# Optimization experiments

Hardware: AMD Instinct MI355X
Metric: run time of the kernel (lower is better)

The kernel has to match this reference:

```python
import jax, jax.numpy as jnp
import numpy as np

B, N, E, H = 2, 2048, 256, 8
D = E // H  # head dim = 32


def setup_inputs() -> dict:
    key = jax.random.key(0)
    ks = jax.random.split(key, 8)
    query_bbox = jax.random.uniform(ks[0], (B, N, 4), dtype=jnp.float32)
    query_feat = jax.random.normal(ks[1], (B, N, E), dtype=jnp.float32)
    s = 1.0 / np.sqrt(E)
    in_proj_w = jax.random.uniform(ks[2], (3 * E, E), minval=-s, maxval=s, dtype=jnp.float32)
    in_proj_b = jax.random.uniform(ks[3], (3 * E,), minval=-s, maxval=s, dtype=jnp.float32)
    out_proj_w = jax.random.uniform(ks[4], (E, E), minval=-s, maxval=s, dtype=jnp.float32)
    out_proj_b = jnp.zeros((E,), dtype=jnp.float32)
    # init_weights(): gen_tau weight zeroed, bias ~ U(0, 2)
    tau_w = jnp.zeros((H, E), dtype=jnp.float32)
    tau_b = jax.random.uniform(ks[5], (H,), minval=0.0, maxval=2.0, dtype=jnp.float32)
    return {
        "query_bbox": query_bbox,
        "query_feat": query_feat,
        "in_proj_w": in_proj_w,
        "in_proj_b": in_proj_b,
        "out_proj_w": out_proj_w,
        "out_proj_b": out_proj_b,
        "tau_w": tau_w,
        "tau_b": tau_b,
    }


def reference(query_bbox, query_feat, in_proj_w, in_proj_b, out_proj_w, out_proj_b, tau_w, tau_b):
    # pairwise center distances, negated; computed under no_grad in torch
    centers = query_bbox[..., :2]                                  # [B,N,2]
    diff = centers[:, :, None, :] - centers[:, None, :, :]         # [B,N,N,2]
    dist = -jnp.sqrt(jnp.sum(diff * diff, axis=-1))                # [B,N,N]
    dist = jax.lax.stop_gradient(dist)

    # per-head tau from query features
    tau = query_feat @ tau_w.T + tau_b                             # [B,N,H]
    tau = jnp.transpose(tau, (0, 2, 1))                            # [B,H,N]
    attn_mask = dist[:, None, :, :] * tau[..., None]               # [B,H,N,N]

    # multi-head self-attention (q = k = v = query_feat)
    qkv = query_feat @ in_proj_w.T + in_proj_b                     # [B,N,3E]
    q, k, v = jnp.split(qkv, 3, axis=-1)
    def heads(x):
        return jnp.transpose(x.reshape(B, N, H, D), (0, 2, 1, 3))  # [B,H,N,D]
    q, k, v = heads(q), heads(k), heads(v)

    scores = jnp.einsum("bhid,bhjd->bhij", q, k) / jnp.sqrt(jnp.float32(D))
    scores = scores + attn_mask
    attn = jax.nn.softmax(scores, axis=-1)                         # [B,H,N,N]
    o = jnp.einsum("bhij,bhjd->bhid", attn, v)                     # [B,H,N,D]
    o = jnp.transpose(o, (0, 2, 1, 3)).reshape(B, N, E)
    out = o @ out_proj_w.T + out_proj_b

    # mmcv MultiheadAttention adds the identity (residual); dropout in eval = id
    return query_feat + out
```

## Files before the change

kernel.cpp:

```cpp
#include <hip/hip_runtime.h>
#include <math.h>

#define BB 2
#define NN 2048
#define EE 256
#define HH 8
#define DD 32

typedef __attribute__((ext_vector_type(8))) short short8;
typedef __attribute__((ext_vector_type(4))) float f32x4;

__device__ inline unsigned short f2bf(float f) {
  union { float f; unsigned int u; } a; a.f = f;
  unsigned int r = a.u + 0x7FFFu + ((a.u >> 16) & 1u);
  return (unsigned short)(r >> 16);
}
__device__ inline float bf2f(short s) {
  union { unsigned int u; float f; } a;
  a.u = ((unsigned int)(unsigned short)s) << 16;
  return a.f;
}

__global__ __launch_bounds__(256) void cast_w_kernel(const float* __restrict__ in_w,
                                                     const float* __restrict__ out_w,
                                                     unsigned short* __restrict__ in_wb,
                                                     unsigned short* __restrict__ out_wb) {
  int i = blockIdx.x * 256 + threadIdx.x;
  float4 v;
  unsigned short* dst;
  if (i < 49152) {
    v = ((const float4*)in_w)[i];
    dst = in_wb + (size_t)i * 4;
  } else {
    v = ((const float4*)out_w)[i - 49152];
    dst = out_wb + (size_t)(i - 49152) * 4;
  }
  ushort4 u;
  u.x = f2bf(v.x); u.y = f2bf(v.y); u.z = f2bf(v.z); u.w = f2bf(v.w);
  *(ushort4*)dst = u;
}

__global__ __launch_bounds__(256) void tau_cxy_kernel(const float* __restrict__ feat,
                                                      const float* __restrict__ tau_w,
                                                      const float* __restrict__ tau_b,
                                                      const float* __restrict__ bbox,
                                                      float* __restrict__ tau2,
                                                      float2* __restrict__ cxy,
                                                      unsigned short* __restrict__ featb) {
  int idx = blockIdx.x * 256 + threadIdx.x;
  int row = idx >> 3, h = idx & 7;
  const float4* f = (const float4*)(feat + (size_t)row * EE);
  const float4* w = (const float4*)(tau_w + (size_t)h * EE);
  float s = 0.f;
#pragma unroll 8
  for (int e = 0; e < EE / 4; ++e) {
    float4 a = f[e], b4 = w[e];
    s = fmaf(a.x, b4.x, s);
    s = fmaf(a.y, b4.y, s);
    s = fmaf(a.z, b4.z, s);
    s = fmaf(a.w, b4.w, s);
    if ((e >> 3) == h) {
      ushort4 u;
      u.x = f2bf(a.x); u.y = f2bf(a.y); u.z = f2bf(a.z); u.w = f2bf(a.w);
      *(ushort4*)(featb + (size_t)row * EE + e * 4) = u;
    }
  }
  tau2[idx] = (s + tau_b[h]) * 1.4426950408889634f;
  if (h == 0) {
    float2 c;
    c.x = bbox[(size_t)row * 4 + 0];
    c.y = bbox[(size_t)row * 4 + 1];
    cxy[row] = c;
  }
}

__global__ __launch_bounds__(256) void dist_kernel(const float2* __restrict__ cxy,
                                                   unsigned short* __restrict__ nds) {
  int bq = blockIdx.x;
  int b = bq >> 7, qt = bq & 127;
  int tid = threadIdx.x;
  int w = tid >> 6, lane = tid & 63;
  int q15 = lane & 15, g = lane >> 4;
  int jt = blockIdx.y * 4 + w;

  float2 ci = cxy[b * NN + qt * 16 + q15];
  const float2* cb = cxy + b * NN + jt * 64;

  float nd[16];
#pragma unroll
  for (int t = 0; t < 4; ++t) {
    float4 c01 = *(const float4*)(cb + t * 16 + g * 4);
    float4 c23 = *(const float4*)(cb + t * 16 + g * 4 + 2);
    float cx[4] = {c01.x, c01.z, c23.x, c23.z};
    float cy[4] = {c01.y, c01.w, c23.y, c23.w};
#pragma unroll
    for (int r = 0; r < 4; ++r) {
      float dx = ci.x - cx[r], dy = ci.y - cy[r];
      nd[t * 4 + r] = -__builtin_amdgcn_sqrtf(fmaf(dy, dy, dx * dx));
    }
  }
  unsigned int u[8];
#pragma unroll
  for (int i = 0; i < 8; ++i)
    asm("v_cvt_pk_bf16_f32 %0, %1, %2" : "=v"(u[i]) : "v"(nd[2 * i]), "v"(nd[2 * i + 1]));
  unsigned short* dst = nds + ((size_t)(b * 128 + qt) * 32 + jt) * 1024 + lane * 16;
  *(uint4*)dst = make_uint4(u[0], u[1], u[2], u[3]);
  *(uint4*)(dst + 8) = make_uint4(u[4], u[5], u[6], u[7]);
}

template <int MODE>
__global__ __launch_bounds__(256) void gemm_mfma_kernel(const unsigned short* __restrict__ Ab,
                                                        const unsigned short* __restrict__ Wb,
                                                        const float* __restrict__ bias,
                                                        const float* __restrict__ resid,
                                                        float* __restrict__ Cf,
                                                        unsigned short* __restrict__ qb,
                                                        unsigned short* __restrict__ kh,
                                                        unsigned short* __restrict__ vpi) {
  int tid = threadIdx.x;
  int wv = tid >> 6, lane = tid & 63;
  int p = lane & 15, g = lane >> 4;
  int mW = blockIdx.y * 64 + wv * 16;
  int nB = blockIdx.x * 64;

  const unsigned short* ap = Ab + (size_t)(mW + p) * 256 + g * 8;
  const unsigned short* wp = Wb + (size_t)(nB + p) * 256 + g * 8;

  f32x4 acc[4] = {{0.f, 0.f, 0.f, 0.f}, {0.f, 0.f, 0.f, 0.f},
                  {0.f, 0.f, 0.f, 0.f}, {0.f, 0.f, 0.f, 0.f}};
#pragma unroll
  for (int kk = 0; kk < 8; ++kk) {
    short8 af = *(const short8*)(ap + kk * 32);
#pragma unroll
    for (int t = 0; t < 4; ++t) {
      short8 wf = *(const short8*)(wp + (size_t)t * 16 * 256 + kk * 32);
      acc[t] = __builtin_amdgcn_mfma_f32_16x16x32_bf16(af, wf, acc[t], 0, 0, 0);
    }
  }

#pragma unroll
  for (int t = 0; t < 4; ++t) {
    int n = nB + t * 16 + p;
    float bn = bias[n];
#pragma unroll
    for (int r = 0; r < 4; ++r) {
      int m = mW + g * 4 + r;
      float v = acc[t][r] + bn;
      if (MODE == 1) {
        Cf[(size_t)m * 256 + n] = v + resid[(size_t)m * 256 + n];
      } else {
        int b = m >> 11, tok = m & 2047;
        if (n < 256) {
          qb[(size_t)m * 256 + n] = f2bf(v * 0.25506659272582955f);
        } else if (n < 512) {
          int h = (n - 256) >> 5, d = n & 31;
          kh[((size_t)(b * 8 + h) * NN + tok) * 32 + d] = f2bf(v);
        } else {
          int h = (n - 512) >> 5, d = n & 31;
          int cp = ((tok & 15) << 1) | ((tok >> 4) & 1);
          vpi[(((size_t)(b * 8 + h) * 64 + (tok >> 5)) * 32 + d) * 32 + cp] = f2bf(v);
        }
      }
    }
  }
}

__global__ __launch_bounds__(256) void attn_kernel(const unsigned short* __restrict__ qb,
                                                   const unsigned short* __restrict__ kh,
                                                   const unsigned short* __restrict__ vpi,
                                                   const unsigned short* __restrict__ nds,
                                                   const float* __restrict__ tau2,
                                                   unsigned short* __restrict__ ob) {
  __shared__ float accT[4][32][17];
  __shared__ float lT[4][16];
  __shared__ float linv[16];

  int bh = blockIdx.y;
  int b = bh >> 3, h = bh & 7;
  int qtb = blockIdx.x;
  int tid = threadIdx.x;
  int w = tid >> 6;
  int lane = tid & 63;
  int q15 = lane & 15, g = lane >> 4;
  int rowq = b * NN + qtb * 16 + q15;

  short8 qf = *(const short8*)(qb + (size_t)rowq * 256 + h * 32 + g * 8);
  float t2 = tau2[(size_t)rowq * HH + h];

  float l = 0.f;
  f32x4 acc0 = {0.f, 0.f, 0.f, 0.f}, acc1 = {0.f, 0.f, 0.f, 0.f};

  const unsigned short* kb = kh + (size_t)bh * NN * 32 + q15 * 32 + g * 8;
  const unsigned short* vb = vpi + (size_t)bh * NN * 32 + q15 * 32 + g * 8;
  const unsigned short* ndb = nds + (size_t)(b * 128 + qtb) * 32 * 1024 + lane * 16;

  int j0base = w * 512;

  short8 kf[2][4];
  short8 vf[2][2];

#pragma unroll
  for (int t = 0; t < 4; ++t)
    kf[0][t] = *(const short8*)(kb + (size_t)(j0base + t * 16) * 32);

#pragma unroll
  for (int tt = 0; tt < 8; ++tt) {
    const int cur = tt & 1, nxt = cur ^ 1;
    const int j0 = j0base + tt * 64;
    const int jt = j0 >> 6;
    if (tt < 7) {
#pragma unroll
      for (int t = 0; t < 4; ++t)
        kf[nxt][t] = *(const short8*)(kb + (size_t)(j0 + 64 + t * 16) * 32);
    }
#pragma unroll
    for (int t2i = 0; t2i < 2; ++t2i)
#pragma unroll
      for (int dh = 0; dh < 2; ++dh)
        vf[t2i][dh] = *(const short8*)(vb + (size_t)((j0 >> 5) + t2i) * 1024 + dh * 512);
    short8 n0 = *(const short8*)(ndb + (size_t)jt * 1024);
    short8 n1 = *(const short8*)(ndb + (size_t)jt * 1024 + 8);
    f32x4 st[4];
#pragma unroll
    for (int t = 0; t < 4; ++t)
      st[t] = __builtin_amdgcn_mfma_f32_16x16x32_bf16(kf[cur][t], qf, (f32x4){0.f, 0.f, 0.f, 0.f}, 0, 0, 0);
    float p[16], lsum = 0.f;
#pragma unroll
    for (int i = 0; i < 16; ++i) {
      float ndf = bf2f(i < 8 ? n0[i] : n1[i - 8]);
      float e = fminf(fmaf(ndf, t2, st[i >> 2][i & 3]), 30.f);
      p[i] = __builtin_amdgcn_exp2f(e);
      lsum += p[i];
    }
    l += lsum;
    union { short8 v; unsigned int u[4]; } pf[2];
#pragma unroll
    for (int t2i = 0; t2i < 2; ++t2i)
#pragma unroll
      for (int wq = 0; wq < 4; ++wq) {
        float lo = p[t2i * 8 + wq];
        float hi = p[t2i * 8 + 4 + wq];
        asm("v_cvt_pk_bf16_f32 %0, %1, %2" : "=v"(pf[t2i].u[wq]) : "v"(lo), "v"(hi));
      }
    acc0 = __builtin_amdgcn_mfma_f32_16x16x32_bf16(vf[0][0], pf[0].v, acc0, 0, 0, 0);
    acc1 = __builtin_amdgcn_mfma_f32_16x16x32_bf16(vf[0][1], pf[0].v, acc1, 0, 0, 0);
    acc0 = __builtin_amdgcn_mfma_f32_16x16x32_bf16(vf[1][0], pf[1].v, acc0, 0, 0, 0);
    acc1 = __builtin_amdgcn_mfma_f32_16x16x32_bf16(vf[1][1], pf[1].v, acc1, 0, 0, 0);
  }

  l += __shfl_xor(l, 16);
  l += __shfl_xor(l, 32);

#pragma unroll
  for (int r = 0; r < 4; ++r) {
    accT[w][g * 4 + r][q15] = acc0[r];
    accT[w][16 + g * 4 + r][q15] = acc1[r];
  }
  if (g == 0) lT[w][q15] = l;
  __syncthreads();

  if (tid < 16) {
    float L = lT[0][tid] + lT[1][tid] + lT[2][tid] + lT[3][tid];
    linv[tid] = 1.f / fmaxf(L, 1e-30f);
  }
  __syncthreads();

#pragma unroll
  for (int ii = 0; ii < 2; ++ii) {
    int i = tid + ii * 256;
    int q = i >> 5, d = i & 31;
    float ov = (accT[0][d][q] + accT[1][d][q] + accT[2][d][q] + accT[3][d][q]) * linv[q];
    ob[((size_t)b * NN + qtb * 16 + q) * EE + h * 32 + d] = f2bf(ov);
  }
}

extern "C" void kernel_launch(void* const* d_in, const int* in_sizes, int n_in,
                              void* d_out, int out_size, void* d_ws, size_t ws_size,
                              hipStream_t stream) {
  const float* bbox  = (const float*)d_in[0];
  const float* feat  = (const float*)d_in[1];
  const float* in_w  = (const float*)d_in[2];
  const float* in_b  = (const float*)d_in[3];
  const float* out_w = (const float*)d_in[4];
  const float* out_b = (const float*)d_in[5];
  const float* tau_w = (const float*)d_in[6];
  const float* tau_b = (const float*)d_in[7];
  float* out = (float*)d_out;

  unsigned short* ob     = (unsigned short*)d_ws;
  unsigned short* featb  = ob + 1048576;
  unsigned short* qb     = featb + 1048576;
  unsigned short* kh     = qb + 1048576;
  unsigned short* vpi    = kh + 1048576;
  unsigned short* in_wb  = vpi + 1048576;
  unsigned short* out_wb = in_wb + 196608;
  float* tau2 = (float*)(out_wb + 65536);
  float2* cxy = (float2*)(tau2 + 32768);
  unsigned short* nds = (unsigned short*)(cxy + 4096);

  cast_w_kernel<<<dim3(256), 256, 0, stream>>>(in_w, out_w, in_wb, out_wb);
  tau_cxy_kernel<<<dim3(128), 256, 0, stream>>>(feat, tau_w, tau_b, bbox, tau2, cxy, featb);
  dist_kernel<<<dim3(BB * 128, 8), 256, 0, stream>>>(cxy, nds);
  gemm_mfma_kernel<0><<<dim3(12, 64), 256, 0, stream>>>(featb, in_wb, in_b, nullptr, nullptr,
                                                        qb, kh, vpi);
  attn_kernel<<<dim3(NN / 16, BB * HH), 256, 0, stream>>>(qb, kh, vpi, nds, tau2, ob);
  gemm_mfma_kernel<1><<<dim3(4, 64), 256, 0, stream>>>(ob, out_wb, out_b, feat, out,
                                                       nullptr, nullptr, nullptr);
}
```

Before: 92.64 us.

## Fuse prep kernels into one launch and process 32 queries per attention block

Three preprocessing kernels (weight cast, tau/feature cast, distance table) are merged into one kernel dispatched by block index, and the distance part now reads bbox centers directly, so the cxy buffer is gone. The attention kernel now handles two 16-query tiles per block, so each K and V fragment loaded is used for twice as many MFMAs, and the block count is halved. This removes two launches and halves K/V traffic per query. In exchange it raises register pressure and LDS use, and gives fewer blocks across the GPU.

```diff
diff --git a/kernel.cpp b/kernel.cpp
--- a/kernel.cpp
+++ b/kernel.cpp
@@ -21,91 +21,85 @@
   return a.f;
 }
 
-__global__ __launch_bounds__(256) void cast_w_kernel(const float* __restrict__ in_w,
-                                                     const float* __restrict__ out_w,
-                                                     unsigned short* __restrict__ in_wb,
-                                                     unsigned short* __restrict__ out_wb) {
-  int i = blockIdx.x * 256 + threadIdx.x;
-  float4 v;
-  unsigned short* dst;
-  if (i < 49152) {
-    v = ((const float4*)in_w)[i];
-    dst = in_wb + (size_t)i * 4;
+__global__ __launch_bounds__(256) void prep_kernel(const float* __restrict__ bbox,
+                                                   const float* __restrict__ feat,
+                                                   const float* __restrict__ in_w,
+                                                   const float* __restrict__ out_w,
+                                                   const float* __restrict__ tau_w,
+                                                   const float* __restrict__ tau_b,
+                                                   unsigned short* __restrict__ in_wb,
+                                                   unsigned short* __restrict__ out_wb,
+                                                   float* __restrict__ tau2,
+                                                   unsigned short* __restrict__ featb,
+                                                   unsigned short* __restrict__ nds) {
+  int blk = blockIdx.x;
+  int tid = threadIdx.x;
+  if (blk < 256) {
+    int i = blk * 256 + tid;
+    float4 v;
+    unsigned short* dst;
+    if (i < 49152) {
+      v = ((const float4*)in_w)[i];
+      dst = in_wb + (size_t)i * 4;
+    } else {
+      v = ((const float4*)out_w)[i - 49152];
+      dst = out_wb + (size_t)(i - 49152) * 4;
+    }
+    ushort4 u;
+    u.x = f2bf(v.x); u.y = f2bf(v.y); u.z = f2bf(v.z); u.w = f2bf(v.w);
+    *(ushort4*)dst = u;
+  } else if (blk < 384) {
+    int idx = (blk - 256) * 256 + tid;
+    int row = idx >> 3, h = idx & 7;
+    const float4* f = (const float4*)(feat + (size_t)row * EE);
+    const float4* w = (const float4*)(tau_w + (size_t)h * EE);
+    float s = 0.f;
+#pragma unroll 8
+    for (int e = 0; e < EE / 4; ++e) {
+      float4 a = f[e], b4 = w[e];
+      s = fmaf(a.x, b4.x, s);
+      s = fmaf(a.y, b4.y, s);
+      s = fmaf(a.z, b4.z, s);
+      s = fmaf(a.w, b4.w, s);
+      if ((e >> 3) == h) {
+        ushort4 u;
+        u.x = f2bf(a.x); u.y = f2bf(a.y); u.z = f2bf(a.z); u.w = f2bf(a.w);
+        *(ushort4*)(featb + (size_t)row * EE + e * 4) = u;
+      }
+    }
+    tau2[idx] = (s + tau_b[h]) * 1.4426950408889634f;
   } else {
-    v = ((const float4*)out_w)[i - 49152];
-    dst = out_wb + (size_t)(i - 49152) * 4;
-  }
-  ushort4 u;
-  u.x = f2bf(v.x); u.y = f2bf(v.y); u.z = f2bf(v.z); u.w = f2bf(v.w);
-  *(ushort4*)dst = u;
-}
-
-__global__ __launch_bounds__(256) void tau_cxy_kernel(const float* __restrict__ feat,
-                                                      const float* __restrict__ tau_w,
-                                                      const float* __restrict__ tau_b,
-                                                      const float* __restrict__ bbox,
-                                                      float* __restrict__ tau2,
-                                                      float2* __restrict__ cxy,
-                                                      unsigned short* __restrict__ featb) {
-  int idx = blockIdx.x * 256 + threadIdx.x;
-  int row = idx >> 3, h = idx & 7;
-  const float4* f = (const float4*)(feat + (size_t)row * EE);
-  const float4* w = (const float4*)(tau_w + (size_t)h * EE);
-  float s = 0.f;
-#pragma unroll 8
-  for (int e = 0; e < EE / 4; ++e) {
-    float4 a = f[e], b4 = w[e];
-    s = fmaf(a.x, b4.x, s);
-    s = fmaf(a.y, b4.y, s);
-    s = fmaf(a.z, b4.z, s);
-    s = fmaf(a.w, b4.w, s);
-    if ((e >> 3) == h) {
-      ushort4 u;
-      u.x = f2bf(a.x); u.y = f2bf(a.y); u.z = f2bf(a.z); u.w = f2bf(a.w);
-      *(ushort4*)(featb + (size_t)row * EE + e * 4) = u;
-    }
-  }
-  tau2[idx] = (s + tau_b[h]) * 1.4426950408889634f;
-  if (h == 0) {
-    float2 c;
-    c.x = bbox[(size_t)row * 4 + 0];
-    c.y = bbox[(size_t)row * 4 + 1];
-    cxy[row] = c;
-  }
-}
-
-__global__ __launch_bounds__(256) void dist_kernel(const float2* __restrict__ cxy,
-                                                   unsigned short* __restrict__ nds) {
-  int bq = blockIdx.x;
-  int b = bq >> 7, qt = bq & 127;
-  int tid = threadIdx.x;
-  int w = tid >> 6, lane = tid & 63;
-  int q15 = lane & 15, g = lane >> 4;
-  int jt = blockIdx.y * 4 + w;
-
-  float2 ci = cxy[b * NN + qt * 16 + q15];
-  const float2* cb = cxy + b * NN + jt * 64;
-
-  float nd[16];
-#pragma unroll
-  for (int t = 0; t < 4; ++t) {
-    float4 c01 = *(const float4*)(cb + t * 16 + g * 4);
-    float4 c23 = *(const float4*)(cb + t * 16 + g * 4 + 2);
-    float cx[4] = {c01.x, c01.z, c23.x, c23.z};
-    float cy[4] = {c01.y, c01.w, c23.y, c23.w};
-#pragma unroll
-    for (int r = 0; r < 4; ++r) {
-      float dx = ci.x - cx[r], dy = ci.y - cy[r];
-      nd[t * 4 + r] = -__builtin_amdgcn_sqrtf(fmaf(dy, dy, dx * dx));
-    }
-  }
-  unsigned int u[8];
-#pragma unroll
-  for (int i = 0; i < 8; ++i)
-    asm("v_cvt_pk_bf16_f32 %0, %1, %2" : "=v"(u[i]) : "v"(nd[2 * i]), "v"(nd[2 * i + 1]));
-  unsigned short* dst = nds + ((size_t)(b * 128 + qt) * 32 + jt) * 1024 + lane * 16;
-  *(uint4*)dst = make_uint4(u[0], u[1], u[2], u[3]);
-  *(uint4*)(dst + 8) = make_uint4(u[4], u[5], u[6], u[7]);
+    int blk2 = blk - 384;
+    int bq = blk2 >> 3;
+    int yy = blk2 & 7;
+    int b = bq >> 7, qt = bq & 127;
+    int w = tid >> 6, lane = tid & 63;
+    int q15 = lane & 15, g = lane >> 4;
+    int jt = yy * 4 + w;
+
+    const float* bi = bbox + (size_t)(b * NN + qt * 16 + q15) * 4;
+    float cix = bi[0], ciy = bi[1];
+    const float* bj = bbox + (size_t)(b * NN + jt * 64) * 4;
+
+    float nd[16];
+#pragma unroll
+    for (int t = 0; t < 4; ++t) {
+#pragma unroll
+      for (int r = 0; r < 4; ++r) {
+        int j = t * 16 + g * 4 + r;
+        float2 cj = *(const float2*)(bj + (size_t)j * 4);
+        float dx = cix - cj.x, dy = ciy - cj.y;
+        nd[t * 4 + r] = -__builtin_amdgcn_sqrtf(fmaf(dy, dy, dx * dx));
+      }
+    }
+    unsigned int u[8];
+#pragma unroll
+    for (int i = 0; i < 8; ++i)
+      asm("v_cvt_pk_bf16_f32 %0, %1, %2" : "=v"(u[i]) : "v"(nd[2 * i]), "v"(nd[2 * i + 1]));
+    unsigned short* dst = nds + ((size_t)(b * 128 + qt) * 32 + jt) * 1024 + lane * 16;
+    *(uint4*)dst = make_uint4(u[0], u[1], u[2], u[3]);
+    *(uint4*)(dst + 8) = make_uint4(u[4], u[5], u[6], u[7]);
+  }
 }
 
 template <int MODE>
@@ -171,9 +165,9 @@
                                                    const unsigned short* __restrict__ nds,
                                                    const float* __restrict__ tau2,
                                                    unsigned short* __restrict__ ob) {
-  __shared__ float accT[4][32][17];
-  __shared__ float lT[4][16];
-  __shared__ float linv[16];
+  __shared__ float accT[4][32][33];
+  __shared__ float lT[4][32];
+  __shared__ float linv[32];
 
   int bh = blockIdx.y;
   int b = bh >> 3, h = bh & 7;
@@ -182,17 +176,23 @@
   int w = tid >> 6;
   int lane = tid & 63;
   int q15 = lane & 15, g = lane >> 4;
-  int rowq = b * NN + qtb * 16 + q15;
-
-  short8 qf = *(const short8*)(qb + (size_t)rowq * 256 + h * 32 + g * 8);
-  float t2 = tau2[(size_t)rowq * HH + h];
-
-  float l = 0.f;
-  f32x4 acc0 = {0.f, 0.f, 0.f, 0.f}, acc1 = {0.f, 0.f, 0.f, 0.f};
+
+  int row0 = b * NN + qtb * 32 + q15;
+  int row1 = row0 + 16;
+
+  short8 qf0 = *(const short8*)(qb + (size_t)row0 * 256 + h * 32 + g * 8);
+  short8 qf1 = *(const short8*)(qb + (size_t)row1 * 256 + h * 32 + g * 8);
+  float t20 = tau2[(size_t)row0 * HH + h];
+  float t21 = tau2[(size_t)row1 * HH + h];
+
+  float l0 = 0.f, l1 = 0.f;
+  f32x4 acc00 = {0.f, 0.f, 0.f, 0.f}, acc01 = {0.f, 0.f, 0.f, 0.f};
+  f32x4 acc10 = {0.f, 0.f, 0.f, 0.f}, acc11 = {0.f, 0.f, 0.f, 0.f};
 
   const unsigned short* kb = kh + (size_t)bh * NN * 32 + q15 * 32 + g * 8;
   const unsigned short* vb = vpi + (size_t)bh * NN * 32 + q15 * 32 + g * 8;
-  const unsigned short* ndb = nds + (size_t)(b * 128 + qtb) * 32 * 1024 + lane * 16;
+  const unsigned short* ndb0 = nds + (size_t)(b * 128 + qtb * 2) * 32768 + lane * 16;
+  const unsigned short* ndb1 = ndb0 + 32768;
 
   int j0base = w * 512;
 
@@ -218,59 +218,82 @@
 #pragma unroll
       for (int dh = 0; dh < 2; ++dh)
         vf[t2i][dh] = *(const short8*)(vb + (size_t)((j0 >> 5) + t2i) * 1024 + dh * 512);
-    short8 n0 = *(const short8*)(ndb + (size_t)jt * 1024);
-    short8 n1 = *(const short8*)(ndb + (size_t)jt * 1024 + 8);
-    f32x4 st[4];
-#pragma unroll
-    for (int t = 0; t < 4; ++t)
-      st[t] = __builtin_amdgcn_mfma_f32_16x16x32_bf16(kf[cur][t], qf, (f32x4){0.f, 0.f, 0.f, 0.f}, 0, 0, 0);
-    float p[16], lsum = 0.f;
+    short8 na0 = *(const short8*)(ndb0 + (size_t)jt * 1024);
+    short8 na1 = *(const short8*)(ndb0 + (size_t)jt * 1024 + 8);
+    short8 nb0 = *(const short8*)(ndb1 + (size_t)jt * 1024);
+    short8 nb1 = *(const short8*)(ndb1 + (size_t)jt * 1024 + 8);
+
+    f32x4 st0[4], st1[4];
+#pragma unroll
+    for (int t = 0; t < 4; ++t) {
+      st0[t] = __builtin_amdgcn_mfma_f32_16x16x32_bf16(kf[cur][t], qf0, (f32x4){0.f, 0.f, 0.f, 0.f}, 0, 0, 0);
+      st1[t] = __builtin_amdgcn_mfma_f32_16x16x32_bf16(kf[cur][t], qf1, (f32x4){0.f, 0.f, 0.f, 0.f}, 0, 0, 0);
+    }
+    float p0[16], p1[16];
+    float ls0 = 0.f, ls1 = 0.f;
 #pragma unroll
     for (int i = 0; i < 16; ++i) {
-      float ndf = bf2f(i < 8 ? n0[i] : n1[i - 8]);
-      float e = fminf(fmaf(ndf, t2, st[i >> 2][i & 3]), 30.f);
-      p[i] = __builtin_amdgcn_exp2f(e);
-      lsum += p[i];
-    }
-    l += lsum;
-    union { short8 v; unsigned int u[4]; } pf[2];
+      float nda = bf2f(i < 8 ? na0[i] : na1[i - 8]);
+      float e0 = fminf(fmaf(nda, t20, st0[i >> 2][i & 3]), 30.f);
+      p0[i] = __builtin_amdgcn_exp2f(e0);
+      ls0 += p0[i];
+      float ndbv = bf2f(i < 8 ? nb0[i] : nb1[i - 8]);
+      float e1 = fminf(fmaf(ndbv, t21, st1[i >> 2][i & 3]), 30.f);
+      p1[i] = __builtin_amdgcn_exp2f(e1);
+      ls1 += p1[i];
+    }
+    l0 += ls0;
+    l1 += ls1;
+    union { short8 v; unsigned int u[4]; } pf0[2], pf1[2];
 #pragma unroll
     for (int t2i = 0; t2i < 2; ++t2i)
 #pragma unroll
       for (int wq = 0; wq < 4; ++wq) {
-        float lo = p[t2i * 8 + wq];
-        float hi = p[t2i * 8 + 4 + wq];
-        asm("v_cvt_pk_bf16_f32 %0, %1, %2" : "=v"(pf[t2i].u[wq]) : "v"(lo), "v"(hi));
+        asm("v_cvt_pk_bf16_f32 %0, %1, %2"
+            : "=v"(pf0[t2i].u[wq]) : "v"(p0[t2i * 8 + wq]), "v"(p0[t2i * 8 + 4 + wq]));
+        asm("v_cvt_pk_bf16_f32 %0, %1, %2"
+            : "=v"(pf1[t2i].u[wq]) : "v"(p1[t2i * 8 + wq]), "v"(p1[t2i * 8 + 4 + wq]));
       }
-    acc0 = __builtin_amdgcn_mfma_f32_16x16x32_bf16(vf[0][0], pf[0].v, acc0, 0, 0, 0);
-    acc1 = __builtin_amdgcn_mfma_f32_16x16x32_bf16(vf[0][1], pf[0].v, acc1, 0, 0, 0);
-    acc0 = __builtin_amdgcn_mfma_f32_16x16x32_bf16(vf[1][0], pf[1].v, acc0, 0, 0, 0);
-    acc1 = __builtin_amdgcn_mfma_f32_16x16x32_bf16(vf[1][1], pf[1].v, acc1, 0, 0, 0);
-  }
-
-  l += __shfl_xor(l, 16);
-  l += __shfl_xor(l, 32);
+    acc00 = __builtin_amdgcn_mfma_f32_16x16x32_bf16(vf[0][0], pf0[0].v, acc00, 0, 0, 0);
+    acc01 = __builtin_amdgcn_mfma_f32_16x16x32_bf16(vf[0][1], pf0[0].v, acc01, 0, 0, 0);
+    acc10 = __builtin_amdgcn_mfma_f32_16x16x32_bf16(vf[0][0], pf1[0].v, acc10, 0, 0, 0);
+    acc11 = __builtin_amdgcn_mfma_f32_16x16x32_bf16(vf[0][1], pf1[0].v, acc11, 0, 0, 0);
+    acc00 = __builtin_amdgcn_mfma_f32_16x16x32_bf16(vf[1][0], pf0[1].v, acc00, 0, 0, 0);
+    acc01 = __builtin_amdgcn_mfma_f32_16x16x32_bf16(vf[1][1], pf0[1].v, acc01, 0, 0, 0);
+    acc10 = __builtin_amdgcn_mfma_f32_16x16x32_bf16(vf[1][0], pf1[1].v, acc10, 0, 0, 0);
+    acc11 = __builtin_amdgcn_mfma_f32_16x16x32_bf16(vf[1][1], pf1[1].v, acc11, 0, 0, 0);
+  }
+
+  l0 += __shfl_xor(l0, 16);
+  l0 += __shfl_xor(l0, 32);
+  l1 += __shfl_xor(l1, 16);
+  l1 += __shfl_xor(l1, 32);
 
 #pragma unroll
   for (int r = 0; r < 4; ++r) {
-    accT[w][g * 4 + r][q15] = acc0[r];
-    accT[w][16 + g * 4 + r][q15] = acc1[r];
-  }
-  if (g == 0) lT[w][q15] = l;
+    accT[w][g * 4 + r][q15] = acc00[r];
+    accT[w][16 + g * 4 + r][q15] = acc01[r];
+    accT[w][g * 4 + r][16 + q15] = acc10[r];
+    accT[w][16 + g * 4 + r][16 + q15] = acc11[r];
+  }
+  if (g == 0) {
+    lT[w][q15] = l0;
+    lT[w][16 + q15] = l1;
+  }
   __syncthreads();
 
-  if (tid < 16) {
+  if (tid < 32) {
     float L = lT[0][tid] + lT[1][tid] + lT[2][tid] + lT[3][tid];
     linv[tid] = 1.f / fmaxf(L, 1e-30f);
   }
   __syncthreads();
 
 #pragma unroll
-  for (int ii = 0; ii < 2; ++ii) {
+  for (int ii = 0; ii < 4; ++ii) {
     int i = tid + ii * 256;
     int q = i >> 5, d = i & 31;
     float ov = (accT[0][d][q] + accT[1][d][q] + accT[2][d][q] + accT[3][d][q]) * linv[q];
-    ob[((size_t)b * NN + qtb * 16 + q) * EE + h * 32 + d] = f2bf(ov);
+    ob[((size_t)b * NN + qtb * 32 + q) * EE + h * 32 + d] = f2bf(ov);
   }
 }
 
@@ -295,15 +318,13 @@
   unsigned short* in_wb  = vpi + 1048576;
   unsigned short* out_wb = in_wb + 196608;
   float* tau2 = (float*)(out_wb + 65536);
-  float2* cxy = (float2*)(tau2 + 32768);
-  unsigned short* nds = (unsigned short*)(cxy + 4096);
-
-  cast_w_kernel<<<dim3(256), 256, 0, stream>>>(in_w, out_w, in_wb, out_wb);
-  tau_cxy_kernel<<<dim3(128), 256, 0, stream>>>(feat, tau_w, tau_b, bbox, tau2, cxy, featb);
-  dist_kernel<<<dim3(BB * 128, 8), 256, 0, stream>>>(cxy, nds);
+  unsigned short* nds = (unsigned short*)(tau2 + 32768);
+
+  prep_kernel<<<dim3(2432), 256, 0, stream>>>(bbox, feat, in_w, out_w, tau_w, tau_b,
+                                              in_wb, out_wb, tau2, featb, nds);
   gemm_mfma_kernel<0><<<dim3(12, 64), 256, 0, stream>>>(featb, in_wb, in_b, nullptr, nullptr,
                                                         qb, kh, vpi);
-  attn_kernel<<<dim3(NN / 16, BB * HH), 256, 0, stream>>>(qb, kh, vpi, nds, tau2, ob);
+  attn_kernel<<<dim3(NN / 32, BB * HH), 256, 0, stream>>>(qb, kh, vpi, nds, tau2, ob);
   gemm_mfma_kernel<1><<<dim3(4, 64), 256, 0, stream>>>(ob, out_wb, out_b, feat, out,
                                                        nullptr, nullptr, nullptr);
 }
```

Measured after the change: 82.27 us, median of 2. 11.2% less time.

## Compute pairwise distances inside attention and merge prep kernels into one launch

Applied to the files above, without the earlier changes.

Removes the separate distance kernel that wrote a bf16 [B,N,N] distance matrix and instead computes the negated center distances on the fly inside the attention loop from the cxy buffer. This drops a large global write plus the matching reads, and also merges the weight-cast and tau/cxy kernels into a single prep launch, removing launches. In exchange the attention kernel does 8x redundant sqrt work (once per head) and extra small loads of centers per tile. Precision changes slightly too, since distances are no longer rounded to bf16.

```diff
diff --git a/kernel.cpp b/kernel.cpp
--- a/kernel.cpp
+++ b/kernel.cpp
@@ -15,97 +15,61 @@
   unsigned int r = a.u + 0x7FFFu + ((a.u >> 16) & 1u);
   return (unsigned short)(r >> 16);
 }
-__device__ inline float bf2f(short s) {
-  union { unsigned int u; float f; } a;
-  a.u = ((unsigned int)(unsigned short)s) << 16;
-  return a.f;
-}
-
-__global__ __launch_bounds__(256) void cast_w_kernel(const float* __restrict__ in_w,
-                                                     const float* __restrict__ out_w,
-                                                     unsigned short* __restrict__ in_wb,
-                                                     unsigned short* __restrict__ out_wb) {
-  int i = blockIdx.x * 256 + threadIdx.x;
-  float4 v;
-  unsigned short* dst;
-  if (i < 49152) {
-    v = ((const float4*)in_w)[i];
-    dst = in_wb + (size_t)i * 4;
+
+__global__ __launch_bounds__(256) void prep_kernel(const float* __restrict__ bbox,
+                                                   const float* __restrict__ feat,
+                                                   const float* __restrict__ in_w,
+                                                   const float* __restrict__ out_w,
+                                                   const float* __restrict__ tau_w,
+                                                   const float* __restrict__ tau_b,
+                                                   unsigned short* __restrict__ in_wb,
+                                                   unsigned short* __restrict__ out_wb,
+                                                   float* __restrict__ tau2,
+                                                   unsigned short* __restrict__ featb,
+                                                   float2* __restrict__ cxy) {
+  int blk = blockIdx.x;
+  int tid = threadIdx.x;
+  if (blk < 256) {
+    int i = blk * 256 + tid;
+    float4 v;
+    unsigned short* dst;
+    if (i < 49152) {
+      v = ((const float4*)in_w)[i];
+      dst = in_wb + (size_t)i * 4;
+    } else {
+      v = ((const float4*)out_w)[i - 49152];
+      dst = out_wb + (size_t)(i - 49152) * 4;
+    }
+    ushort4 u;
+    u.x = f2bf(v.x); u.y = f2bf(v.y); u.z = f2bf(v.z); u.w = f2bf(v.w);
+    *(ushort4*)dst = u;
   } else {
-    v = ((const float4*)out_w)[i - 49152];
-    dst = out_wb + (size_t)(i - 49152) * 4;
-  }
-  ushort4 u;
-  u.x = f2bf(v.x); u.y = f2bf(v.y); u.z = f2bf(v.z); u.w = f2bf(v.w);
-  *(ushort4*)dst = u;
-}
-
-__global__ __launch_bounds__(256) void tau_cxy_kernel(const float* __restrict__ feat,
-                                                      const float* __restrict__ tau_w,
-                                                      const float* __restrict__ tau_b,
-                                                      const float* __restrict__ bbox,
-                                                      float* __restrict__ tau2,
-                                                      float2* __restrict__ cxy,
-                                                      unsigned short* __restrict__ featb) {
-  int idx = blockIdx.x * 256 + threadIdx.x;
-  int row = idx >> 3, h = idx & 7;
-  const float4* f = (const float4*)(feat + (size_t)row * EE);
-  const float4* w = (const float4*)(tau_w + (size_t)h * EE);
-  float s = 0.f;
+    int idx = (blk - 256) * 256 + tid;
+    int row = idx >> 3, h = idx & 7;
+    const float4* f = (const float4*)(feat + (size_t)row * EE);
+    const float4* w = (const float4*)(tau_w + (size_t)h * EE);
+    float s = 0.f;
 #pragma unroll 8
-  for (int e = 0; e < EE / 4; ++e) {
-    float4 a = f[e], b4 = w[e];
-    s = fmaf(a.x, b4.x, s);
-    s = fmaf(a.y, b4.y, s);
-    s = fmaf(a.z, b4.z, s);
-    s = fmaf(a.w, b4.w, s);
-    if ((e >> 3) == h) {
-      ushort4 u;
-      u.x = f2bf(a.x); u.y = f2bf(a.y); u.z = f2bf(a.z); u.w = f2bf(a.w);
-      *(ushort4*)(featb + (size_t)row * EE + e * 4) = u;
-    }
-  }
-  tau2[idx] = (s + tau_b[h]) * 1.4426950408889634f;
-  if (h == 0) {
-    float2 c;
-    c.x = bbox[(size_t)row * 4 + 0];
-    c.y = bbox[(size_t)row * 4 + 1];
-    cxy[row] = c;
-  }
-}
-
-__global__ __launch_bounds__(256) void dist_kernel(const float2* __restrict__ cxy,
-                                                   unsigned short* __restrict__ nds) {
-  int bq = blockIdx.x;
-  int b = bq >> 7, qt = bq & 127;
-  int tid = threadIdx.x;
-  int w = tid >> 6, lane = tid & 63;
-  int q15 = lane & 15, g = lane >> 4;
-  int jt = blockIdx.y * 4 + w;
-
-  float2 ci = cxy[b * NN + qt * 16 + q15];
-  const float2* cb = cxy + b * NN + jt * 64;
-
-  float nd[16];
-#pragma unroll
-  for (int t = 0; t < 4; ++t) {
-    float4 c01 = *(const float4*)(cb + t * 16 + g * 4);
-    float4 c23 = *(const float4*)(cb + t * 16 + g * 4 + 2);
-    float cx[4] = {c01.x, c01.z, c23.x, c23.z};
-    float cy[4] = {c01.y, c01.w, c23.y, c23.w};
-#pragma unroll
-    for (int r = 0; r < 4; ++r) {
-      float dx = ci.x - cx[r], dy = ci.y - cy[r];
-      nd[t * 4 + r] = -__builtin_amdgcn_sqrtf(fmaf(dy, dy, dx * dx));
-    }
-  }
-  unsigned int u[8];
-#pragma unroll
-  for (int i = 0; i < 8; ++i)
-    asm("v_cvt_pk_bf16_f32 %0, %1, %2" : "=v"(u[i]) : "v"(nd[2 * i]), "v"(nd[2 * i + 1]));
-  unsigned short* dst = nds + ((size_t)(b * 128 + qt) * 32 + jt) * 1024 + lane * 16;
-  *(uint4*)dst = make_uint4(u[0], u[1], u[2], u[3]);
-  *(uint4*)(dst + 8) = make_uint4(u[4], u[5], u[6], u[7]);
+    for (int e = 0; e < EE / 4; ++e) {
+      float4 a = f[e], b4 = w[e];
+      s = fmaf(a.x, b4.x, s);
+      s = fmaf(a.y, b4.y, s);
+      s = fmaf(a.z, b4.z, s);
+      s = fmaf(a.w, b4.w, s);
+      if ((e >> 3) == h) {
+        ushort4 u;
+        u.x = f2bf(a.x); u.y = f2bf(a.y); u.z = f2bf(a.z); u.w = f2bf(a.w);
+        *(ushort4*)(featb + (size_t)row * EE + e * 4) = u;
+      }
+    }
+    tau2[idx] = (s + tau_b[h]) * 1.4426950408889634f;
+    if (h == 0) {
+      float2 c;
+      c.x = bbox[(size_t)row * 4 + 0];
+      c.y = bbox[(size_t)row * 4 + 1];
+      cxy[row] = c;
+    }
+  }
 }
 
 template <int MODE>
@@ -168,16 +132,16 @@
 __global__ __launch_bounds__(256) void attn_kernel(const unsigned short* __restrict__ qb,
                                                    const unsigned short* __restrict__ kh,
                                                    const unsigned short* __restrict__ vpi,
-                                                   const unsigned short* __restrict__ nds,
+                                                   const float2* __restrict__ cxy,
                                                    const float* __restrict__ tau2,
                                                    unsigned short* __restrict__ ob) {
   __shared__ float accT[4][32][17];
   __shared__ float lT[4][16];
   __shared__ float linv[16];
 
+  int qtb = blockIdx.x;
   int bh = blockIdx.y;
   int b = bh >> 3, h = bh & 7;
-  int qtb = blockIdx.x;
   int tid = threadIdx.x;
   int w = tid >> 6;
   int lane = tid & 63;
@@ -186,13 +150,14 @@
 
   short8 qf = *(const short8*)(qb + (size_t)rowq * 256 + h * 32 + g * 8);
   float t2 = tau2[(size_t)rowq * HH + h];
+  float2 ci = cxy[rowq];
 
   float l = 0.f;
   f32x4 acc0 = {0.f, 0.f, 0.f, 0.f}, acc1 = {0.f, 0.f, 0.f, 0.f};
 
   const unsigned short* kb = kh + (size_t)bh * NN * 32 + q15 * 32 + g * 8;
   const unsigned short* vb = vpi + (size_t)bh * NN * 32 + q15 * 32 + g * 8;
-  const unsigned short* ndb = nds + (size_t)(b * 128 + qtb) * 32 * 1024 + lane * 16;
+  const float2* cb = cxy + b * NN;
 
   int j0base = w * 512;
 
@@ -207,7 +172,6 @@
   for (int tt = 0; tt < 8; ++tt) {
     const int cur = tt & 1, nxt = cur ^ 1;
     const int j0 = j0base + tt * 64;
-    const int jt = j0 >> 6;
     if (tt < 7) {
 #pragma unroll
       for (int t = 0; t < 4; ++t)
@@ -218,19 +182,26 @@
 #pragma unroll
       for (int dh = 0; dh < 2; ++dh)
         vf[t2i][dh] = *(const short8*)(vb + (size_t)((j0 >> 5) + t2i) * 1024 + dh * 512);
-    short8 n0 = *(const short8*)(ndb + (size_t)jt * 1024);
-    short8 n1 = *(const short8*)(ndb + (size_t)jt * 1024 + 8);
     f32x4 st[4];
 #pragma unroll
     for (int t = 0; t < 4; ++t)
       st[t] = __builtin_amdgcn_mfma_f32_16x16x32_bf16(kf[cur][t], qf, (f32x4){0.f, 0.f, 0.f, 0.f}, 0, 0, 0);
     float p[16], lsum = 0.f;
 #pragma unroll
-    for (int i = 0; i < 16; ++i) {
-      float ndf = bf2f(i < 8 ? n0[i] : n1[i - 8]);
-      float e = fminf(fmaf(ndf, t2, st[i >> 2][i & 3]), 30.f);
-      p[i] = __builtin_amdgcn_exp2f(e);
-      lsum += p[i];
+    for (int t = 0; t < 4; ++t) {
+      float4 c01 = *(const float4*)(cb + j0 + t * 16 + g * 4);
+      float4 c23 = *(const float4*)(cb + j0 + t * 16 + g * 4 + 2);
+      float cx[4] = {c01.x, c01.z, c23.x, c23.z};
+      float cy[4] = {c01.y, c01.w, c23.y, c23.w};
+#pragma unroll
+      for (int r = 0; r < 4; ++r) {
+        float dx = ci.x - cx[r], dy = ci.y - cy[r];
+        float nd = -__builtin_amdgcn_sqrtf(fmaf(dy, dy, dx * dx));
+        float e = fminf(fmaf(nd, t2, st[t][r]), 30.f);
+        float pv = __builtin_amdgcn_exp2f(e);
+        p[t * 4 + r] = pv;
+        lsum += pv;
+      }
     }
     l += lsum;
     union { short8 v; unsigned int u[4]; } pf[2];
@@ -238,9 +209,8 @@
     for (int t2i = 0; t2i < 2; ++t2i)
 #pragma unroll
       for (int wq = 0; wq < 4; ++wq) {
-        float lo = p[t2i * 8 + wq];
-        float hi = p[t2i * 8 + 4 + wq];
-        asm("v_cvt_pk_bf16_f32 %0, %1, %2" : "=v"(pf[t2i].u[wq]) : "v"(lo), "v"(hi));
+        asm("v_cvt_pk_bf16_f32 %0, %1, %2"
+            : "=v"(pf[t2i].u[wq]) : "v"(p[t2i * 8 + wq]), "v"(p[t2i * 8 + 4 + wq]));
       }
     acc0 = __builtin_amdgcn_mfma_f32_16x16x32_bf16(vf[0][0], pf[0].v, acc0, 0, 0, 0);
     acc1 = __builtin_amdgcn_mfma_f32_16x16x32_bf16(vf[0][1], pf[0].v, acc1, 0, 0, 0);
@@ -296,14 +266,12 @@
   unsigned short* out_wb = in_wb + 196608;
   float* tau2 = (float*)(out_wb + 65536);
   float2* cxy = (float2*)(tau2 + 32768);
-  unsigned short* nds = (unsigned short*)(cxy + 4096);
-
-  cast_w_kernel<<<dim3(256), 256, 0, stream>>>(in_w, out_w, in_wb, out_wb);
-  tau_cxy_kernel<<<dim3(128), 256, 0, stream>>>(feat, tau_w, tau_b, bbox, tau2, cxy, featb);
-  dist_kernel<<<dim3(BB * 128, 8), 256, 0, stream>>>(cxy, nds);
+
+  prep_kernel<<<dim3(384), 256, 0, stream>>>(bbox, feat, in_w, out_w, tau_w, tau_b,
+                                             in_wb, out_wb, tau2, featb, cxy);
   gemm_mfma_kernel<0><<<dim3(12, 64), 256, 0, stream>>>(featb, in_wb, in_b, nullptr, nullptr,
                                                         qb, kh, vpi);
-  attn_kernel<<<dim3(NN / 16, BB * HH), 256, 0, stream>>>(qb, kh, vpi, nds, tau2, ob);
+  attn_kernel<<<dim3(NN / 16, BB * HH), 256, 0, stream>>>(qb, kh, vpi, cxy, tau2, ob);
   gemm_mfma_kernel<1><<<dim3(4, 64), 256, 0, stream>>>(ob, out_wb, out_b, feat, out,
                                                        nullptr, nullptr, nullptr);
 }
```

Result: no change. 92.09 us (-0.6%).
